# Optimization experiments

Hardware: AMD Instinct MI355X
Metric: run time of the kernel (lower is better)

Reference implementation:

```python
import jax, jax.numpy as jnp
import numpy as np

HIDDEN = 2048
Q_HEADS = 16
KV_HEADS = 4
HEAD_DIM = HIDDEN // Q_HEADS  # 128
GROUPS = Q_HEADS // KV_HEADS  # 4


def setup_inputs() -> dict:
    key = jax.random.key(0)
    ks = jax.random.split(key, 5)
    scale = 1.0 / np.sqrt(HIDDEN)
    x = jax.random.normal(ks[0], (1, 4096, HIDDEN), dtype=jnp.float32)
    # nn.Linear weights stored as [out_features, in_features]
    Wq = jax.random.uniform(ks[1], (Q_HEADS * HEAD_DIM, HIDDEN), jnp.float32, -scale, scale)
    Wk = jax.random.uniform(ks[2], (KV_HEADS * HEAD_DIM, HIDDEN), jnp.float32, -scale, scale)
    Wv = jax.random.uniform(ks[3], (KV_HEADS * HEAD_DIM, HIDDEN), jnp.float32, -scale, scale)
    Wo = jax.random.uniform(ks[4], (HIDDEN, HIDDEN), jnp.float32, -scale, scale)
    return {"x": x, "Wq": Wq, "Wk": Wk, "Wv": Wv, "Wo": Wo}


def reference(x, Wq, Wk, Wv, Wo):
    b, s, _ = x.shape
    norm = jnp.asarray(np.sqrt(HEAD_DIM), x.dtype)
    # Projections (Linear without bias: x @ W.T)
    q = (x @ Wq.T).reshape(b, s, KV_HEADS, GROUPS, HEAD_DIM)  # group q heads by shared kv head
    k = (x @ Wk.T).reshape(b, s, KV_HEADS, HEAD_DIM)
    v = (x @ Wv.T).reshape(b, s, KV_HEADS, HEAD_DIM)
    # Scores: repeat_interleave of KV is equivalent to sharing k across the g axis
    att = jnp.einsum('bskgd,btkd->bkgst', q, k) / norm  # [b,kv,groups,s,s]
    att = jax.nn.softmax(att, axis=-1)
    out = jnp.einsum('bkgst,btkd->bskgd', att, v).reshape(b, s, HIDDEN)
    return out @ Wo.T
```

## Files before the change

kernel.cpp:

```cpp
#include <hip/hip_runtime.h>
#include <stdint.h>

#define SEQ 4096
#define HID 2048

typedef __attribute__((ext_vector_type(8))) short short8;
typedef __attribute__((ext_vector_type(4))) float f32x4;
typedef unsigned int u32;

__device__ __forceinline__ short bf16_rne(float f) {
  u32 u = __builtin_bit_cast(u32, f);
  u += 0x7FFFu + ((u >> 16) & 1u);
  return (short)(u >> 16);
}

__device__ __forceinline__ void gload16(const void* gp, void* lp) {
  __builtin_amdgcn_global_load_lds(
      (const __attribute__((address_space(1))) u32*)(uintptr_t)gp,
      (__attribute__((address_space(3))) u32*)(uintptr_t)lp, 16, 0, 0);
}

__global__ __launch_bounds__(256) void cast_bf16(const float* __restrict__ in,
                                                 short* __restrict__ out, int n8) {
  int i = blockIdx.x * 256 + threadIdx.x;
  if (i >= n8) return;
  const f32x4* p = (const f32x4*)in + (size_t)i * 2;
  f32x4 a = p[0], b = p[1];
  short8 o;
#pragma unroll
  for (int j = 0; j < 4; ++j) { o[j] = bf16_rne(a[j]); o[j + 4] = bf16_rne(b[j]); }
  *((short8*)out + i) = o;
}

__global__ __launch_bounds__(256) void transpose_v(const short* __restrict__ qkv,
                                                   short* __restrict__ vt) {
  __shared__ __align__(16) short tile[64][72];
  int rb = blockIdx.x * 64, cb = blockIdx.y * 64;
  int tid = threadIdx.x;
  int tr = tid >> 3, tc = (tid & 7) * 8;
#pragma unroll
  for (int i = 0; i < 2; ++i)
    *(short8*)&tile[tr + i * 32][tc] =
        *(const short8*)&qkv[(size_t)(rb + tr + i * 32) * 3072 + 2560 + cb + tc];
  __syncthreads();
#pragma unroll
  for (int i = 0; i < 2; ++i) {
    int c = tr + i * 32;
    short8 v;
#pragma unroll
    for (int j = 0; j < 8; ++j) {
      int pos = tc + j;
      int p = pos & 31, ch = pos >> 5;
      int tl = ch * 32 + (p >> 1) + (p & 1) * 16;
      v[j] = tile[tl][c];
    }
    *(short8*)&vt[(size_t)(cb + c) * SEQ + rb + tc] = v;
  }
}

template <typename CT>
__global__ __launch_bounds__(256, 2) void gemm_nt(const short* __restrict__ A,
                                                  const short* __restrict__ B,
                                                  CT* __restrict__ C, int M, int N, int K) {
  __shared__ __align__(16) short As[128 * 32];
  __shared__ __align__(16) short Bs[128 * 32];
  int tid = threadIdx.x, wave = tid >> 6, lane = tid & 63;
  int lr = lane & 15, lg = lane >> 4;
  int wr = wave >> 1, wc = wave & 1;
  size_t rowA0 = (size_t)blockIdx.y * 128, colB0 = (size_t)blockIdx.x * 128;
  f32x4 acc[4][4] = {};

  for (int kt = 0; kt < K; kt += 32) {
#pragma unroll
    for (int c = 0; c < 2; ++c) {
      int chunk = wave * 2 + c;
      int row = chunk * 16 + (lane >> 2);
      int col = (lane & 3) * 8;
      gload16(A + (rowA0 + row) * (size_t)K + kt + col, &As[chunk * 512]);
      gload16(B + (colB0 + row) * (size_t)K + kt + col, &Bs[chunk * 512]);
    }
    __syncthreads();
    short8 a[4], b[4];
#pragma unroll
    for (int i = 0; i < 4; ++i) {
      a[i] = *(const short8*)&As[(wr * 64 + i * 16 + lr) * 32 + lg * 8];
      b[i] = *(const short8*)&Bs[(wc * 64 + i * 16 + lr) * 32 + lg * 8];
    }
#pragma unroll
    for (int i = 0; i < 4; ++i)
#pragma unroll
      for (int j = 0; j < 4; ++j)
        acc[i][j] = __builtin_amdgcn_mfma_f32_16x16x32_bf16(a[i], b[j], acc[i][j], 0, 0, 0);
    __syncthreads();
  }
#pragma unroll
  for (int i = 0; i < 4; ++i)
#pragma unroll
    for (int j = 0; j < 4; ++j)
#pragma unroll
      for (int r = 0; r < 4; ++r) {
        size_t row = rowA0 + wr * 64 + i * 16 + lg * 4 + r;
        size_t col = colB0 + wc * 64 + j * 16 + lr;
        if constexpr (sizeof(CT) == 2) C[row * N + col] = (CT)bf16_rne(acc[i][j][r]);
        else C[row * N + col] = acc[i][j][r];
      }
}

__global__ __launch_bounds__(256, 4) void attn_kernel(const short* __restrict__ QKV,
                                                      const short* __restrict__ Vt,
                                                      short* __restrict__ Oat) {
  __shared__ __align__(16) short Ks[2][32 * 128];
  __shared__ __align__(16) short Vs[2][32 * 128];
  __shared__ __align__(16) u32 Ps[4][16 * 16];
  int tid = threadIdx.x, wave = tid >> 6, lane = tid & 63;
  int lr = lane & 15, lg = lane >> 4;
  int h = blockIdx.y, kv = h >> 2;
  int q0 = blockIdx.x * 64 + wave * 16;

  short8 qf[4];
#pragma unroll
  for (int ks = 0; ks < 4; ++ks)
    qf[ks] = *(const short8*)&QKV[(size_t)(q0 + lr) * 3072 + h * 128 + ks * 32 + lg * 8];

  f32x4 oacc[8] = {};
  float m_run[4], lsum[4];
#pragma unroll
  for (int r = 0; r < 4; ++r) { m_run[r] = -1e30f; lsum[r] = 0.f; }

  const float sc = 1.44269504089f * 0.08838834764831845f;
  const float THR_S = 60.f;
  const short* Kbase = QKV + 2048 + kv * 128;
  const short* Vbase = Vt + (size_t)(kv * 128) * SEQ;

  auto stageK = [&](int b, int t0) {
#pragma unroll
    for (int c = 0; c < 2; ++c) {
      int chunk = wave * 2 + c;
      int row = chunk * 4 + lg;
      int colb = (lr * 16) ^ ((row & 7) << 4);
      gload16(Kbase + (size_t)(t0 + row) * 3072 + colb / 2, &Ks[b][chunk * 512]);
    }
  };
  auto stageV = [&](int b, int t0) {
#pragma unroll
    for (int c = 0; c < 2; ++c) {
      int chunk = wave * 2 + c;
      int r = chunk * 4 + lg;
      int lb = (lr * 16) ^ ((r & 7) << 4);
      int d = r * 4 + (lb >> 6);
      gload16(Vbase + (size_t)d * SEQ + t0 + ((lb & 63) >> 1), &Vs[b][chunk * 512]);
    }
  };

  stageK(0, 0);
  stageV(0, 0);
  __syncthreads();
  int buf = 0;

  for (int t0 = 0; t0 < SEQ; t0 += 32) {
    int tn = (t0 + 32 < SEQ) ? t0 + 32 : 0;
    stageK(buf ^ 1, tn);
    stageV(buf ^ 1, tn);

    f32x4 sacc[2] = {};
    __builtin_amdgcn_s_setprio(1);
#pragma unroll
    for (int ks = 0; ks < 4; ++ks) {
      short8 kf[2];
#pragma unroll
      for (int ct = 0; ct < 2; ++ct) {
        int trow = ct * 16 + lr;
        int cb = (ks * 64 + lg * 16) ^ ((trow & 7) << 4);
        kf[ct] = *(const short8*)&Ks[buf][trow * 128 + cb / 2];
      }
#pragma unroll
      for (int ct = 0; ct < 2; ++ct)
        sacc[ct] = __builtin_amdgcn_mfma_f32_16x16x32_bf16(qf[ks], kf[ct], sacc[ct], 0, 0, 0);
    }
    __builtin_amdgcn_s_setprio(0);

    float vmax[4];
    int need = 0;
#pragma unroll
    for (int r = 0; r < 4; ++r) {
      vmax[r] = fmaxf(sacc[0][r], sacc[1][r]);
      need |= (vmax[r] > m_run[r] + THR_S) ? 1 : 0;
    }
    if (__any(need)) {
#pragma unroll
      for (int r = 0; r < 4; ++r) {
        float v = vmax[r];
        v = fmaxf(v, __shfl_xor(v, 1));
        v = fmaxf(v, __shfl_xor(v, 2));
        v = fmaxf(v, __shfl_xor(v, 4));
        v = fmaxf(v, __shfl_xor(v, 8));
        float mnew = fmaxf(m_run[r], v);
        float corr = __builtin_amdgcn_exp2f((m_run[r] - mnew) * sc);
        lsum[r] *= corr;
        m_run[r] = mnew;
#pragma unroll
        for (int db = 0; db < 8; ++db) oacc[db][r] *= corr;
      }
    }
#pragma unroll
    for (int r = 0; r < 4; ++r) {
      float p0 = __builtin_amdgcn_exp2f((sacc[0][r] - m_run[r]) * sc);
      float p1 = __builtin_amdgcn_exp2f((sacc[1][r] - m_run[r]) * sc);
      lsum[r] += p0 + p1;
      u32 pk;
      asm("v_cvt_pk_bf16_f32 %0, %1, %2" : "=v"(pk) : "v"(p0), "v"(p1));
      Ps[wave][(lg * 4 + r) * 16 + lr] = pk;
    }

    short8 pa = *(const short8*)&Ps[wave][lr * 16 + lg * 4];
    __builtin_amdgcn_s_setprio(1);
#pragma unroll
    for (int db = 0; db < 8; ++db) {
      int d = db * 16 + lr;
      int r = d >> 2;
      int lb = ((d & 3) * 64 + lg * 16) ^ ((r & 7) << 4);
      short8 bv = *(const short8*)&Vs[buf][r * 128 + lb / 2];
      oacc[db] = __builtin_amdgcn_mfma_f32_16x16x32_bf16(pa, bv, oacc[db], 0, 0, 0);
    }
    __builtin_amdgcn_s_setprio(0);

    __syncthreads();
    buf ^= 1;
  }

#pragma unroll
  for (int r = 0; r < 4; ++r) {
    float s = lsum[r];
    s += __shfl_xor(s, 1);
    s += __shfl_xor(s, 2);
    s += __shfl_xor(s, 4);
    s += __shfl_xor(s, 8);
    lsum[r] = s;
  }
#pragma unroll
  for (int db = 0; db < 8; ++db)
#pragma unroll
    for (int r = 0; r < 4; ++r) {
      size_t row = q0 + lg * 4 + r;
      size_t col = h * 128 + db * 16 + lr;
      Oat[row * HID + col] = bf16_rne(oacc[db][r] / lsum[r]);
    }
}

extern "C" void kernel_launch(void* const* d_in, const int* in_sizes, int n_in,
                              void* d_out, int out_size, void* d_ws, size_t ws_size,
                              hipStream_t stream) {
  const float* x = (const float*)d_in[0];
  const float* Wq = (const float*)d_in[1];
  const float* Wk = (const float*)d_in[2];
  const float* Wv = (const float*)d_in[3];
  const float* Wo = (const float*)d_in[4];
  float* out = (float*)d_out;
  char* ws = (char*)d_ws;

  short* xb = (short*)(ws);
  short* wqkv = (short*)(ws + (16u << 20));
  short* wob = (short*)(ws + (28u << 20));
  short* qkv = (short*)(ws + (36u << 20));
  short* vt = wqkv;
  short* oat = xb;

  cast_bf16<<<4096, 256, 0, stream>>>(x, xb, 1048576);
  cast_bf16<<<2048, 256, 0, stream>>>(Wq, wqkv, 524288);
  cast_bf16<<<512, 256, 0, stream>>>(Wk, wqkv + (size_t)2048 * 2048, 131072);
  cast_bf16<<<512, 256, 0, stream>>>(Wv, wqkv + (size_t)2560 * 2048, 131072);
  cast_bf16<<<2048, 256, 0, stream>>>(Wo, wob, 524288);

  gemm_nt<short><<<dim3(24, 32), 256, 0, stream>>>(xb, wqkv, qkv, 4096, 3072, 2048);
  transpose_v<<<dim3(64, 8), 256, 0, stream>>>(qkv, vt);
  attn_kernel<<<dim3(64, 16), 256, 0, stream>>>(qkv, vt, oat);
  gemm_nt<float><<<dim3(16, 32), 256, 0, stream>>>(oat, wob, out, 4096, HID, 2048);
}
```

Baseline: 331.4 us.

## Rewrite attention with 32x32x16 MFMA, S-transposed layout and register P exchange

New measurement: 294.2 us. 1.13x faster.

```diff
diff --git a/kernel.cpp b/kernel.cpp
--- a/kernel.cpp
+++ b/kernel.cpp
@@ -6,7 +6,9 @@
 
 typedef __attribute__((ext_vector_type(8))) short short8;
 typedef __attribute__((ext_vector_type(4))) float f32x4;
+typedef __attribute__((ext_vector_type(16))) float f32x16;
 typedef unsigned int u32;
+typedef __attribute__((ext_vector_type(4))) u32 u32x4;
 
 __device__ __forceinline__ short bf16_rne(float f) {
   u32 u = __builtin_bit_cast(u32, f);
@@ -48,12 +50,7 @@
     int c = tr + i * 32;
     short8 v;
 #pragma unroll
-    for (int j = 0; j < 8; ++j) {
-      int pos = tc + j;
-      int p = pos & 31, ch = pos >> 5;
-      int tl = ch * 32 + (p >> 1) + (p & 1) * 16;
-      v[j] = tile[tl][c];
-    }
+    for (int j = 0; j < 8; ++j) v[j] = tile[tc + j][c];
     *(short8*)&vt[(size_t)(cb + c) * SEQ + rb + tc] = v;
   }
 }
@@ -106,49 +103,41 @@
       }
 }
 
-__global__ __launch_bounds__(256, 4) void attn_kernel(const short* __restrict__ QKV,
+__global__ __launch_bounds__(256, 2) void attn_kernel(const short* __restrict__ QKV,
                                                       const short* __restrict__ Vt,
                                                       short* __restrict__ Oat) {
-  __shared__ __align__(16) short Ks[2][32 * 128];
-  __shared__ __align__(16) short Vs[2][32 * 128];
-  __shared__ __align__(16) u32 Ps[4][16 * 16];
+  __shared__ __align__(16) short Ks[2][4096];
+  __shared__ __align__(16) short Vs[2][4096];
   int tid = threadIdx.x, wave = tid >> 6, lane = tid & 63;
-  int lr = lane & 15, lg = lane >> 4;
+  int l31 = lane & 31, hi = lane >> 5;
   int h = blockIdx.y, kv = h >> 2;
-  int q0 = blockIdx.x * 64 + wave * 16;
-
-  short8 qf[4];
-#pragma unroll
-  for (int ks = 0; ks < 4; ++ks)
-    qf[ks] = *(const short8*)&QKV[(size_t)(q0 + lr) * 3072 + h * 128 + ks * 32 + lg * 8];
-
-  f32x4 oacc[8] = {};
-  float m_run[4], lsum[4];
-#pragma unroll
-  for (int r = 0; r < 4; ++r) { m_run[r] = -1e30f; lsum[r] = 0.f; }
+  int q0 = blockIdx.x * 128 + wave * 32;
+
+  short8 qf[8];
+#pragma unroll
+  for (int kb = 0; kb < 8; ++kb)
+    qf[kb] = *(const short8*)&QKV[(size_t)(q0 + l31) * 3072 + h * 128 + kb * 16 + hi * 8];
+
+  f32x16 oacc[4] = {};
+  float m_run = -1e30f, lsum = 0.f;
 
   const float sc = 1.44269504089f * 0.08838834764831845f;
   const float THR_S = 60.f;
   const short* Kbase = QKV + 2048 + kv * 128;
-  const short* Vbase = Vt + (size_t)(kv * 128) * SEQ;
 
   auto stageK = [&](int b, int t0) {
 #pragma unroll
-    for (int c = 0; c < 2; ++c) {
-      int chunk = wave * 2 + c;
-      int row = chunk * 4 + lg;
-      int colb = (lr * 16) ^ ((row & 7) << 4);
-      gload16(Kbase + (size_t)(t0 + row) * 3072 + colb / 2, &Ks[b][chunk * 512]);
+    for (int cc = 0; cc < 2; ++cc) {
+      int c = wave * 2 + cc;
+      gload16(Kbase + (size_t)(t0 + l31) * 3072 + c * 16 + hi * 8, &Ks[b][c * 512]);
     }
   };
   auto stageV = [&](int b, int t0) {
 #pragma unroll
-    for (int c = 0; c < 2; ++c) {
-      int chunk = wave * 2 + c;
-      int r = chunk * 4 + lg;
-      int lb = (lr * 16) ^ ((r & 7) << 4);
-      int d = r * 4 + (lb >> 6);
-      gload16(Vbase + (size_t)d * SEQ + t0 + ((lb & 63) >> 1), &Vs[b][chunk * 512]);
+    for (int cc = 0; cc < 2; ++cc) {
+      int c = wave * 2 + cc;
+      int d = (c & 1) * 64 + lane;
+      gload16(Vt + (size_t)(kv * 128 + d) * SEQ + t0 + (c >> 1) * 8, &Vs[b][c * 512]);
     }
   };
 
@@ -162,65 +151,60 @@
     stageK(buf ^ 1, tn);
     stageV(buf ^ 1, tn);
 
-    f32x4 sacc[2] = {};
+    f32x16 sacc = {};
     __builtin_amdgcn_s_setprio(1);
 #pragma unroll
-    for (int ks = 0; ks < 4; ++ks) {
-      short8 kf[2];
-#pragma unroll
-      for (int ct = 0; ct < 2; ++ct) {
-        int trow = ct * 16 + lr;
-        int cb = (ks * 64 + lg * 16) ^ ((trow & 7) << 4);
-        kf[ct] = *(const short8*)&Ks[buf][trow * 128 + cb / 2];
-      }
-#pragma unroll
-      for (int ct = 0; ct < 2; ++ct)
-        sacc[ct] = __builtin_amdgcn_mfma_f32_16x16x32_bf16(qf[ks], kf[ct], sacc[ct], 0, 0, 0);
+    for (int kb = 0; kb < 8; ++kb) {
+      short8 kf = *(const short8*)&Ks[buf][((kb * 2 + hi) * 32 + l31) * 8];
+      sacc = __builtin_amdgcn_mfma_f32_32x32x16_bf16(kf, qf[kb], sacc, 0, 0, 0);
     }
     __builtin_amdgcn_s_setprio(0);
 
-    float vmax[4];
-    int need = 0;
-#pragma unroll
-    for (int r = 0; r < 4; ++r) {
-      vmax[r] = fmaxf(sacc[0][r], sacc[1][r]);
-      need |= (vmax[r] > m_run[r] + THR_S) ? 1 : 0;
-    }
-    if (__any(need)) {
-#pragma unroll
-      for (int r = 0; r < 4; ++r) {
-        float v = vmax[r];
-        v = fmaxf(v, __shfl_xor(v, 1));
-        v = fmaxf(v, __shfl_xor(v, 2));
-        v = fmaxf(v, __shfl_xor(v, 4));
-        v = fmaxf(v, __shfl_xor(v, 8));
-        float mnew = fmaxf(m_run[r], v);
-        float corr = __builtin_amdgcn_exp2f((m_run[r] - mnew) * sc);
-        lsum[r] *= corr;
-        m_run[r] = mnew;
-#pragma unroll
-        for (int db = 0; db < 8; ++db) oacc[db][r] *= corr;
-      }
-    }
-#pragma unroll
-    for (int r = 0; r < 4; ++r) {
-      float p0 = __builtin_amdgcn_exp2f((sacc[0][r] - m_run[r]) * sc);
-      float p1 = __builtin_amdgcn_exp2f((sacc[1][r] - m_run[r]) * sc);
-      lsum[r] += p0 + p1;
-      u32 pk;
-      asm("v_cvt_pk_bf16_f32 %0, %1, %2" : "=v"(pk) : "v"(p0), "v"(p1));
-      Ps[wave][(lg * 4 + r) * 16 + lr] = pk;
-    }
-
-    short8 pa = *(const short8*)&Ps[wave][lr * 16 + lg * 4];
+    float vmax = fmaxf(sacc[0], sacc[1]);
+#pragma unroll
+    for (int r = 2; r < 16; ++r) vmax = fmaxf(vmax, sacc[r]);
+    if (__any(vmax > m_run + THR_S)) {
+      float mnew = fmaxf(fmaxf(vmax, __shfl_xor(vmax, 32)), m_run);
+      float corr = __builtin_amdgcn_exp2f((m_run - mnew) * sc);
+      lsum *= corr;
+      m_run = mnew;
+#pragma unroll
+      for (int nb = 0; nb < 4; ++nb) oacc[nb] *= corr;
+    }
+
+    float p[16];
+    float ps = 0.f;
+#pragma unroll
+    for (int r = 0; r < 16; ++r) {
+      p[r] = __builtin_amdgcn_exp2f((sacc[r] - m_run) * sc);
+      ps += p[r];
+    }
+    lsum += ps;
+    u32 w[8];
+#pragma unroll
+    for (int i = 0; i < 8; ++i)
+      asm("v_cvt_pk_bf16_f32 %0, %1, %2" : "=v"(w[i]) : "v"(p[2 * i]), "v"(p[2 * i + 1]));
+
+    u32 W[8];
+#pragma unroll
+    for (int i = 0; i < 2; ++i) {
+      u32 ex = __shfl_xor(hi ? w[i] : w[i + 2], 32);
+      W[i] = hi ? ex : w[i];
+      W[i + 2] = hi ? w[i + 2] : ex;
+      u32 ex2 = __shfl_xor(hi ? w[i + 4] : w[i + 6], 32);
+      W[i + 4] = hi ? ex2 : w[i + 4];
+      W[i + 6] = hi ? w[i + 6] : ex2;
+    }
+    short8 pa0 = __builtin_bit_cast(short8, (u32x4){W[0], W[1], W[2], W[3]});
+    short8 pa1 = __builtin_bit_cast(short8, (u32x4){W[4], W[5], W[6], W[7]});
+
     __builtin_amdgcn_s_setprio(1);
 #pragma unroll
-    for (int db = 0; db < 8; ++db) {
-      int d = db * 16 + lr;
-      int r = d >> 2;
-      int lb = ((d & 3) * 64 + lg * 16) ^ ((r & 7) << 4);
-      short8 bv = *(const short8*)&Vs[buf][r * 128 + lb / 2];
-      oacc[db] = __builtin_amdgcn_mfma_f32_16x16x32_bf16(pa, bv, oacc[db], 0, 0, 0);
+    for (int nb = 0; nb < 4; ++nb) {
+      short8 v0 = *(const short8*)&Vs[buf][((hi)*128 + nb * 32 + l31) * 8];
+      oacc[nb] = __builtin_amdgcn_mfma_f32_32x32x16_bf16(pa0, v0, oacc[nb], 0, 0, 0);
+      short8 v1 = *(const short8*)&Vs[buf][((2 + hi) * 128 + nb * 32 + l31) * 8];
+      oacc[nb] = __builtin_amdgcn_mfma_f32_32x32x16_bf16(pa1, v1, oacc[nb], 0, 0, 0);
     }
     __builtin_amdgcn_s_setprio(0);
 
@@ -228,23 +212,16 @@
     buf ^= 1;
   }
 
-#pragma unroll
-  for (int r = 0; r < 4; ++r) {
-    float s = lsum[r];
-    s += __shfl_xor(s, 1);
-    s += __shfl_xor(s, 2);
-    s += __shfl_xor(s, 4);
-    s += __shfl_xor(s, 8);
-    lsum[r] = s;
-  }
-#pragma unroll
-  for (int db = 0; db < 8; ++db)
-#pragma unroll
-    for (int r = 0; r < 4; ++r) {
-      size_t row = q0 + lg * 4 + r;
-      size_t col = h * 128 + db * 16 + lr;
-      Oat[row * HID + col] = bf16_rne(oacc[db][r] / lsum[r]);
-    }
+  lsum += __shfl_xor(lsum, 32);
+  float linv = 1.f / lsum;
+#pragma unroll
+  for (int r = 0; r < 16; ++r) {
+    int qrow = (r & 3) + 8 * (r >> 2) + 4 * hi;
+    float lr_ = __shfl(linv, qrow);
+#pragma unroll
+    for (int nb = 0; nb < 4; ++nb)
+      Oat[(size_t)(q0 + qrow) * HID + h * 128 + nb * 32 + l31] = bf16_rne(oacc[nb][r] * lr_);
+  }
 }
 
 extern "C" void kernel_launch(void* const* d_in, const int* in_sizes, int n_in,
@@ -273,6 +250,6 @@
 
   gemm_nt<short><<<dim3(24, 32), 256, 0, stream>>>(xb, wqkv, qkv, 4096, 3072, 2048);
   transpose_v<<<dim3(64, 8), 256, 0, stream>>>(qkv, vt);
-  attn_kernel<<<dim3(64, 16), 256, 0, stream>>>(qkv, vt, oat);
+  attn_kernel<<<dim3(32, 16), 256, 0, stream>>>(qkv, vt, oat);
   gemm_nt<float><<<dim3(16, 32), 256, 0, stream>>>(oat, wob, out, 4096, HID, 2048);
 }
```
